# Optimization experiments

Measured on AMD Instinct MI355X. Metric: run time of the kernel, lower is better.

## Reference

```python
import jax, jax.numpy as jnp
import numpy as np

B, G, T, N = 2, 4, 64, 300
D = 256          # detr_dim == feature_dim
R = 4            # ffn_dim_ratio
MD = 32          # motion_dim


def _xavier(key, shape):
    lim = (6.0 / (shape[0] + shape[1])) ** 0.5
    return jax.random.uniform(key, shape, jnp.float32, -lim, lim)


def setup_inputs() -> dict:
    key = jax.random.key(0)
    ks = jax.random.split(key, 16)
    feats = jax.random.normal(ks[0], (B, G, T, N, D), jnp.float32)
    boxes = jax.random.uniform(ks[1], (B, G, T, N, 4), jnp.float32)
    masks = jax.random.bernoulli(ks[2], 0.3, (B, G, T, N))
    # per-trajectory permutation of frame ids 0..T-1 (unique -> unambiguous scatter)
    u = jax.random.uniform(ks[3], (B, G, N, T))
    times = jnp.swapaxes(jnp.argsort(u, axis=-1).astype(jnp.int32), 2, 3)  # [B,G,T,N]
    return {
        'trajectory_features': feats,
        'trajectory_boxes': boxes,
        'trajectory_masks': masks,
        'trajectory_times': times,
        'adp_w1': _xavier(ks[4], (D, D * R)), 'adp_b1': jnp.zeros((D * R,), jnp.float32),
        'adp_w2': _xavier(ks[5], (D * R, D)), 'adp_b2': jnp.zeros((D,), jnp.float32),
        'norm_g': jnp.ones((D,), jnp.float32), 'norm_b': jnp.zeros((D,), jnp.float32),
        'mot_w1': _xavier(ks[6], (12, MD // 2)), 'mot_b1': jnp.zeros((MD // 2,), jnp.float32),
        'mot_w2': _xavier(ks[7], (MD // 2, MD)), 'mot_b2': jnp.zeros((MD,), jnp.float32),
        'fus_w1': _xavier(ks[8], (D + MD, D)), 'fus_b1': jnp.zeros((D,), jnp.float32),
        'fus_w2': _xavier(ks[9], (D, D)), 'fus_b2': jnp.zeros((D,), jnp.float32),
        'ffn_w1': _xavier(ks[10], (D, D * R)), 'ffn_b1': jnp.zeros((D * R,), jnp.float32),
        'ffn_w2': _xavier(ks[11], (D * R, D)), 'ffn_b2': jnp.zeros((D,), jnp.float32),
        'fnorm_g': jnp.ones((D,), jnp.float32), 'fnorm_b': jnp.zeros((D,), jnp.float32),
    }


def _ffn(x, w1, b1, w2, b2):
    return jax.nn.gelu(x @ w1 + b1, approximate=False) @ w2 + b2


def _ln(x, g, b):
    m = x.mean(-1, keepdims=True)
    v = ((x - m) ** 2).mean(-1, keepdims=True)
    return (x - m) / jnp.sqrt(v + 1e-5) * g + b


def _motion_features(boxes, masks, times, mot_w1, mot_b1, mot_w2, mot_b2):
    # boxes [B,G,T,N,4] -> trajectory-major [B,G,N,T,*]
    b_, g_, t_, n_ = masks.shape
    md = mot_b2.shape[0]
    bx = jnp.swapaxes(boxes, 2, 3)              # [B,G,N,T,4]
    valid = ~jnp.swapaxes(masks, 2, 3)          # [B,G,N,T]
    tm = jnp.swapaxes(times, 2, 3)              # [B,G,N,T]
    # sort valid entries first, by time (stable)
    order = jnp.argsort(jnp.where(valid, tm, t_ + 1), axis=-1)
    sb = jnp.take_along_axis(bx, order[..., None], axis=3)   # sorted boxes
    st = jnp.take_along_axis(tm, order, axis=-1)             # sorted times
    cnt = valid.sum(-1)                                      # [B,G,N]
    pos = jnp.arange(t_)
    in_count = pos[None, None, None, :] < cnt[..., None]
    dt = jnp.maximum(st - jnp.roll(st, 1, axis=-1), 1).astype(sb.dtype)[..., None]
    mask_v = ((pos >= 1)[None, None, None, :] & in_count)[..., None]
    vel = jnp.where(mask_v, (sb - jnp.roll(sb, 1, axis=3)) / dt, 0.0)
    mask_a = ((pos >= 2)[None, None, None, :] & in_count)[..., None]
    acc = jnp.where(mask_a, (vel - jnp.roll(vel, 1, axis=3)) / dt, 0.0)
    mv = jnp.concatenate([sb, vel, acc], axis=-1)            # [B,G,N,T,12]
    enc = jax.nn.gelu(mv @ mot_w1 + mot_b1, approximate=False) @ mot_w2 + mot_b2
    write = in_count & (cnt >= 2)[..., None] & (st < t_)
    frame = jnp.where(write, st, t_)                         # t_ -> dropped
    bi, gi, ni, ti = jnp.meshgrid(jnp.arange(b_), jnp.arange(g_), jnp.arange(n_),
                                  jnp.arange(t_), indexing='ij')
    out = jnp.zeros((b_, g_, t_, n_, md), sb.dtype)
    return out.at[bi, gi, frame, ni].set(enc, mode='drop')


def reference(trajectory_features, trajectory_boxes, trajectory_masks, trajectory_times,
              adp_w1, adp_b1, adp_w2, adp_b2, norm_g, norm_b,
              mot_w1, mot_b1, mot_w2, mot_b2,
              fus_w1, fus_b1, fus_w2, fus_b2,
              ffn_w1, ffn_b1, ffn_w2, ffn_b2, fnorm_g, fnorm_b):
    x = trajectory_features + _ffn(trajectory_features, adp_w1, adp_b1, adp_w2, adp_b2)
    x = _ln(x, norm_g, norm_b)
    motion = _motion_features(trajectory_boxes, trajectory_masks, trajectory_times,
                              mot_w1, mot_b1, mot_w2, mot_b2)
    cat = jnp.concatenate([x, motion], axis=-1)
    fused = jax.nn.gelu(cat @ fus_w1 + fus_b1, approximate=False) @ fus_w2 + fus_b2
    fused = fused + _ffn(fused, ffn_w1, ffn_b1, ffn_w2, ffn_b2)
    fused = _ln(fused, fnorm_g, fnorm_b)
    return fused, motion
```

## Files before the change

### kernel.cpp

```cpp
#include <hip/hip_runtime.h>

typedef __bf16 bf16x8 __attribute__((ext_vector_type(8)));
typedef __bf16 bf16x4 __attribute__((ext_vector_type(4)));
typedef float f32x4 __attribute__((ext_vector_type(4)));

namespace {

constexpr int T_ = 64;
constexpr int N_ = 300;
constexpr int MD_ = 32;
constexpr int BG_ = 8;
constexpr long MROWS_ = (long)BG_ * T_ * N_;
constexpr long FUSED_N = MROWS_ * 256;
constexpr int MB = 32;

constexpr long PA1 = 0;
constexpr long PA2 = 262144;
constexpr long PF1 = 524288;
constexpr long PF2 = 598016;
constexpr long PN1 = 663552;
constexpr long PN2 = 925696;

__device__ __forceinline__ float gelu_f(float x) {
  const float x2 = x * x;
  const float z2 = x * fmaf(x2, 0.07135481627f, 1.5957691216f);
  const float t = __builtin_amdgcn_rcpf(1.0f + __expf(z2));
  return x * (1.0f - t);
}

__device__ __forceinline__ float gelu_exact(float x) {
  return 0.5f * x * (1.0f + erff(x * 0.7071067811865476f));
}

__global__ void k_zero_flag(int* f) { *f = 0; }

__global__ void k_detect_mask(const unsigned char* __restrict__ m, int nbytes,
                              int* __restrict__ f) {
  int i = blockIdx.x * 256 + threadIdx.x;
  if (i < nbytes && (i & 3) != 0 && m[i] != 0) atomicOr(f, 1);
}

__global__ __launch_bounds__(256)
void k_motion(const float* __restrict__ boxes, const void* __restrict__ masks,
              const int* __restrict__ times,
              const float* __restrict__ mw1, const float* __restrict__ mb1,
              const float* __restrict__ mw2, const float* __restrict__ mb2,
              float* __restrict__ motion, const int* __restrict__ flagp) {
  __shared__ int slot[4][T_];
  __shared__ int sts[4][T_];
  __shared__ float sbx[4][T_][4];
  __shared__ float otile[4][T_][MD_];
  const int tid = threadIdx.x;
  const int w = tid >> 6, l = tid & 63;
  const int traj = blockIdx.x * 4 + w;
  const int bg = traj / N_, n = traj - bg * N_;
  const int isbool = *flagp;
  const long idx = ((long)bg * T_ + l) * N_ + n;
  const bool msk = isbool ? (((const unsigned char*)masks)[idx] != 0)
                          : (((const int*)masks)[idx] != 0);
  const bool valid = !msk;
  const int tm = times[idx];

  slot[w][l] = -1;
  sts[w][l] = 0;
  *(float4*)&sbx[w][l][0] = make_float4(0.f, 0.f, 0.f, 0.f);
  __syncthreads();
  if (valid) slot[w][tm] = l;
  __syncthreads();

  const int ot = slot[w][l];
  const bool vp = ot >= 0;
  const unsigned long long bal = __ballot(vp);
  const int cnt = __builtin_popcountll(bal);
  const int pos = __builtin_popcountll(bal & ((1ull << l) - 1ull));
  if (vp) {
    sts[w][pos] = l;
    const float4 bx = *(const float4*)(boxes + (((long)bg * T_ + ot) * N_ + n) * 4);
    *(float4*)&sbx[w][pos][0] = bx;
  }
  __syncthreads();

  const int stp = sts[w][l];
  const int stm1 = sts[w][(l + 63) & 63];
  const float4 sb = *(const float4*)&sbx[w][l][0];
  const float4 sbm = *(const float4*)&sbx[w][(l + 63) & 63][0];
  const float dt = (float)max(stp - stm1, 1);
  const float inv = 1.0f / dt;
  const bool okv = (l >= 1) && (l < cnt);
  float v0 = okv ? (sb.x - sbm.x) * inv : 0.f;
  float v1 = okv ? (sb.y - sbm.y) * inv : 0.f;
  float v2 = okv ? (sb.z - sbm.z) * inv : 0.f;
  float v3 = okv ? (sb.w - sbm.w) * inv : 0.f;
  const float p0 = __shfl_up(v0, 1, 64);
  const float p1 = __shfl_up(v1, 1, 64);
  const float p2 = __shfl_up(v2, 1, 64);
  const float p3 = __shfl_up(v3, 1, 64);
  const bool oka = (l >= 2) && (l < cnt);
  const float a0 = oka ? (v0 - p0) * inv : 0.f;
  const float a1 = oka ? (v1 - p1) * inv : 0.f;
  const float a2 = oka ? (v2 - p2) * inv : 0.f;
  const float a3 = oka ? (v3 - p3) * inv : 0.f;

  const float mv[12] = {sb.x, sb.y, sb.z, sb.w, v0, v1, v2, v3, a0, a1, a2, a3};
  float e1[16];
#pragma unroll
  for (int i = 0; i < 16; ++i) {
    float a = mb1[i];
#pragma unroll
    for (int c = 0; c < 12; ++c) a = fmaf(mv[c], mw1[c * 16 + i], a);
    e1[i] = gelu_exact(a);
  }
  float enc[32];
#pragma unroll
  for (int o = 0; o < 32; ++o) {
    float a = mb2[o];
#pragma unroll
    for (int i = 0; i < 16; ++i) a = fmaf(e1[i], mw2[i * 32 + o], a);
    enc[o] = a;
  }

#pragma unroll
  for (int c = 0; c < 32; c += 4)
    *(float4*)&otile[w][l][c] = make_float4(0.f, 0.f, 0.f, 0.f);
  __syncthreads();
  if (l < cnt && cnt >= 2) {
#pragma unroll
    for (int c = 0; c < 32; ++c) otile[w][stp][c] = enc[c];
  }
  __syncthreads();

  float* mbase = motion + ((long)bg * T_ * N_ + n) * MD_;
  const float4* srcv = (const float4*)&otile[w][l][0];
  float4* dstv = (float4*)(mbase + (long)l * N_ * MD_);
#pragma unroll
  for (int q = 0; q < 8; ++q) dstv[q] = srcv[q];
}

__global__ void k_pack(const float* __restrict__ W, __bf16* __restrict__ P,
                       int K, int NN) {
  int gid = blockIdx.x * 256 + threadIdx.x;
  int total = (K >> 5) * (NN >> 4) * 64;
  if (gid >= total) return;
  int l = gid & 63, f = gid >> 6;
  int NT = NN >> 4;
  int kb = f / NT, nt = f - kb * NT;
  int krow = kb * 32 + (l >> 4) * 8;
  int col = nt * 16 + (l & 15);
  bf16x8 v;
#pragma unroll
  for (int e = 0; e < 8; ++e) v[e] = (__bf16)W[(long)(krow + e) * NN + col];
  *(bf16x8*)(P + (long)gid * 8) = v;
}

template <int NKB, bool MOT, int NT>
__device__ __forceinline__ void produce_chunk(
    const char* regA, const char* regM, char* hb, const __bf16* pb1,
    const float* b1, int r, int wid, int l, int lr, int lk) {
  const int nt = r * 4 + wid;
  f32x4 t[2];
  {
    const float4 bv = *(const float4*)(b1 + r * 64 + wid * 16 + lk * 4);
#pragma unroll
    for (int rt = 0; rt < 2; ++rt) t[rt] = f32x4{bv.x, bv.y, bv.z, bv.w};
  }
  const __bf16* wp = pb1 + ((long)nt << 9) + (l << 3);
  bf16x8 w0 = *(const bf16x8*)(wp);
  bf16x8 w1 = w0;
  if (NKB > 1) w1 = *(const bf16x8*)(wp + ((long)NT << 9));
#pragma unroll
  for (int kb = 0; kb < NKB; ++kb) {
    const bf16x8 wf = (kb & 1) ? w1 : w0;
    if (kb + 2 < NKB) {
      const bf16x8 v = *(const bf16x8*)(wp + ((long)(kb + 2) * NT << 9));
      if (kb & 1) w1 = v; else w0 = v;
    }
    __builtin_amdgcn_s_setprio(1);
#pragma unroll
    for (int rt = 0; rt < 2; ++rt) {
      const int row = rt * 16 + lr;
      bf16x8 xf;
      if (MOT && kb == NKB - 1)
        xf = *(const bf16x8*)(regM + row * 64 + ((lk ^ (row & 3)) << 4));
      else
        xf = *(const bf16x8*)(regA + row * 512 +
                              ((((kb << 2) + lk) ^ (row & 7)) << 4));
      t[rt] = __builtin_amdgcn_mfma_f32_16x16x32_bf16(wf, xf, t[rt], 0, 0, 0);
    }
    __builtin_amdgcn_s_setprio(0);
  }
#pragma unroll
  for (int rt = 0; rt < 2; ++rt) {
    const int row = rt * 16 + lr;
    bf16x4 hv;
#pragma unroll
    for (int e = 0; e < 4; ++e) hv[e] = (__bf16)gelu_f(t[rt][e]);
    *(bf16x4*)(hb + row * 128 + ((wid * 32 + lk * 8) ^ ((row & 7) << 4))) = hv;
  }
}

__device__ __forceinline__ void consume_chunk(const char* hb,
                                              const __bf16* pb2, int kbg0,
                                              int l, int lr, int lk, int wn,
                                              f32x4 (&acc)[2][4]) {
  const __bf16* wp = pb2 + ((long)(kbg0 * 16 + wn * 4) << 9) + (l << 3);
#pragma unroll
  for (int kbl = 0; kbl < 2; ++kbl) {
    bf16x8 bw[4];
#pragma unroll
    for (int j = 0; j < 4; ++j)
      bw[j] = *(const bf16x8*)(wp + ((long)(kbl * 16 + j) << 9));
    bf16x8 a[2];
#pragma unroll
    for (int m = 0; m < 2; ++m) {
      const int row = m * 16 + lr;
      a[m] = *(const bf16x8*)(hb + row * 128 +
                              ((kbl * 64 + lk * 16) ^ ((row & 7) << 4)));
    }
    __builtin_amdgcn_s_setprio(1);
#pragma unroll
    for (int j = 0; j < 4; ++j)
#pragma unroll
      for (int m = 0; m < 2; ++m)
        acc[m][j] = __builtin_amdgcn_mfma_f32_16x16x32_bf16(a[m], bw[j],
                                                            acc[m][j], 0, 0, 0);
    __builtin_amdgcn_s_setprio(0);
  }
}

__global__ __launch_bounds__(256, 4)
void k_mfma(const float* __restrict__ feats, const float* __restrict__ motion,
            const __bf16* __restrict__ pw,
            const float* __restrict__ ba1, const float* __restrict__ ba2,
            const float* __restrict__ ng, const float* __restrict__ nb,
            const float* __restrict__ bf1, const float* __restrict__ bf2,
            const float* __restrict__ bn1, const float* __restrict__ bn2,
            const float* __restrict__ fg, const float* __restrict__ fb,
            float* __restrict__ out) {
  __shared__ __align__(16) char smem[27648];
  char* regA = smem;
  char* hb0 = smem + 16384;
  char* hb1 = smem + 20480;
  char* regM = smem + 24576;
  float* redp = (float*)(smem + 26624);

  const int tid = threadIdx.x;
  const int l = tid & 63, wid = tid >> 6;
  const int lr = l & 15, lk = l >> 4;
  const int wn = wid;
  const int colb = wn * 64;
  const long rowbase = (long)blockIdx.x * MB;

  const __bf16* pa1 = pw + PA1;
  const __bf16* pa2 = pw + PA2;
  const __bf16* pf1 = pw + PF1;
  const __bf16* pf2 = pw + PF2;
  const __bf16* pn1 = pw + PN1;
  const __bf16* pn2 = pw + PN2;

  auto ln_stats = [&](const f32x4 (&acc)[2][4], float (&mean)[2][4],
                      float (&rstd)[2][4]) {
    float s1[2][4], s2[2][4];
#pragma unroll
    for (int m = 0; m < 2; ++m)
#pragma unroll
      for (int e = 0; e < 4; ++e) { s1[m][e] = 0.f; s2[m][e] = 0.f; }
#pragma unroll
    for (int m = 0; m < 2; ++m)
#pragma unroll
      for (int j = 0; j < 4; ++j)
#pragma unroll
        for (int e = 0; e < 4; ++e) {
          s1[m][e] += acc[m][j][e];
          s2[m][e] += acc[m][j][e] * acc[m][j][e];
        }
#pragma unroll
    for (int o = 1; o < 16; o <<= 1)
#pragma unroll
      for (int m = 0; m < 2; ++m)
#pragma unroll
        for (int e = 0; e < 4; ++e) {
          s1[m][e] += __shfl_xor(s1[m][e], o);
          s2[m][e] += __shfl_xor(s2[m][e], o);
        }
    if (lr == 0) {
#pragma unroll
      for (int m = 0; m < 2; ++m)
#pragma unroll
        for (int e = 0; e < 4; ++e) {
          const int row = m * 16 + lk * 4 + e;
          redp[(row * 4 + wn) * 2 + 0] = s1[m][e];
          redp[(row * 4 + wn) * 2 + 1] = s2[m][e];
        }
    }
    __syncthreads();
#pragma unroll
    for (int m = 0; m < 2; ++m)
#pragma unroll
      for (int e = 0; e < 4; ++e) {
        const int row = m * 16 + lk * 4 + e;
        const float S1 = redp[(row * 4 + 0) * 2] + redp[(row * 4 + 1) * 2] +
                         redp[(row * 4 + 2) * 2] + redp[(row * 4 + 3) * 2];
        const float S2 = redp[(row * 4 + 0) * 2 + 1] + redp[(row * 4 + 1) * 2 + 1] +
                         redp[(row * 4 + 2) * 2 + 1] + redp[(row * 4 + 3) * 2 + 1];
        const float mu = S1 * (1.0f / 256.0f);
        const float var = S2 * (1.0f / 256.0f) - mu * mu;
        mean[m][e] = mu;
        rstd[m][e] = rsqrtf(var + 1e-5f);
      }
  };

  f32x4 acc2[2][4];
#pragma unroll
  for (int j = 0; j < 4; ++j) {
    const int col = colb + j * 16 + lr;
    const float bv = ba2[col];
#pragma unroll
    for (int m = 0; m < 2; ++m)
#pragma unroll
      for (int e = 0; e < 4; ++e) {
        const int row = m * 16 + lk * 4 + e;
        acc2[m][j][e] = bv + feats[(rowbase + row) * 256 + col];
      }
  }
#pragma unroll
  for (int it = 0; it < 4; ++it) {
    const int c = tid + it * 256;
    const int row = c >> 5, cc = c & 31;
    const float* src = feats + (rowbase + row) * 256 + cc * 8;
    bf16x8 v;
#pragma unroll
    for (int e = 0; e < 8; ++e) v[e] = (__bf16)src[e];
    *(bf16x8*)(regA + row * 512 + ((cc ^ (row & 7)) << 4)) = v;
  }
  __syncthreads();

  produce_chunk<8, false, 64>(regA, regM, hb0, pa1, ba1, 0, wid, l, lr, lk);
  __syncthreads();
#pragma unroll 1
  for (int r = 0; r < 16; ++r) {
    if (r < 15)
      produce_chunk<8, false, 64>(regA, regM, ((r + 1) & 1) ? hb1 : hb0, pa1,
                                  ba1, r + 1, wid, l, lr, lk);
    consume_chunk((r & 1) ? hb1 : hb0, pa2, r * 2, l, lr, lk, wn, acc2);
    __syncthreads();
  }

  {
    float mean[2][4], rstd[2][4];
    ln_stats(acc2, mean, rstd);
#pragma unroll
    for (int j = 0; j < 4; ++j) {
      const int col = colb + j * 16 + lr;
      const float gv = ng[col], bv = nb[col];
#pragma unroll
      for (int m = 0; m < 2; ++m)
#pragma unroll
        for (int e = 0; e < 4; ++e) {
          const int row = m * 16 + lk * 4 + e;
          const float v = (acc2[m][j][e] - mean[m][e]) * rstd[m][e] * gv + bv;
          *(__bf16*)(regA + row * 512 + (((col >> 3) ^ (row & 7)) << 4) +
                     ((col & 7) << 1)) = (__bf16)v;
        }
    }
    if (tid < 128) {
      const int row = tid >> 2, cc = tid & 3;
      const float* src = motion + (rowbase + row) * 32 + cc * 8;
      bf16x8 v;
#pragma unroll
      for (int e = 0; e < 8; ++e) v[e] = (__bf16)src[e];
      *(bf16x8*)(regM + row * 64 + ((cc ^ (row & 3)) << 4)) = v;
    }
  }
  __syncthreads();

  {
#pragma unroll
    for (int j = 0; j < 4; ++j) {
      const float bv = bf2[colb + j * 16 + lr];
#pragma unroll
      for (int m = 0; m < 2; ++m) acc2[m][j] = {bv, bv, bv, bv};
    }
    produce_chunk<9, true, 16>(regA, regM, hb0, pf1, bf1, 0, wid, l, lr, lk);
    __syncthreads();
#pragma unroll 1
    for (int r = 0; r < 4; ++r) {
      if (r < 3)
        produce_chunk<9, true, 16>(regA, regM, ((r + 1) & 1) ? hb1 : hb0, pf1,
                                   bf1, r + 1, wid, l, lr, lk);
      consume_chunk((r & 1) ? hb1 : hb0, pf2, r * 2, l, lr, lk, wn, acc2);
      __syncthreads();
    }
#pragma unroll
    for (int j = 0; j < 4; ++j) {
      const int col = colb + j * 16 + lr;
      const float bv = bn2[col];
#pragma unroll
      for (int m = 0; m < 2; ++m)
#pragma unroll
        for (int e = 0; e < 4; ++e) {
          const int row = m * 16 + lk * 4 + e;
          const float fv = acc2[m][j][e];
          *(__bf16*)(regA + row * 512 + (((col >> 3) ^ (row & 7)) << 4) +
                     ((col & 7) << 1)) = (__bf16)fv;
          acc2[m][j][e] = fv + bv;
        }
    }
  }
  __syncthreads();

  produce_chunk<8, false, 64>(regA, regM, hb0, pn1, bn1, 0, wid, l, lr, lk);
  __syncthreads();
#pragma unroll 1
  for (int r = 0; r < 16; ++r) {
    if (r < 15)
      produce_chunk<8, false, 64>(regA, regM, ((r + 1) & 1) ? hb1 : hb0, pn1,
                                  bn1, r + 1, wid, l, lr, lk);
    consume_chunk((r & 1) ? hb1 : hb0, pn2, r * 2, l, lr, lk, wn, acc2);
    __syncthreads();
  }

  {
    float mean[2][4], rstd[2][4];
    ln_stats(acc2, mean, rstd);
#pragma unroll
    for (int j = 0; j < 4; ++j) {
      const int col = colb + j * 16 + lr;
      const float gv = fg[col], bv = fb[col];
#pragma unroll
      for (int m = 0; m < 2; ++m)
#pragma unroll
        for (int e = 0; e < 4; ++e) {
          const int row = m * 16 + lk * 4 + e;
          out[(rowbase + row) * 256 + col] =
              (acc2[m][j][e] - mean[m][e]) * rstd[m][e] * gv + bv;
        }
    }
  }
}

}

extern "C" void kernel_launch(void* const* d_in, const int* in_sizes, int n_in,
                              void* d_out, int out_size, void* d_ws, size_t ws_size,
                              hipStream_t stream) {
  const float* feats = (const float*)d_in[0];
  const float* boxes = (const float*)d_in[1];
  const void*  masks = d_in[2];
  const int*   times = (const int*)d_in[3];
  const float* wa1 = (const float*)d_in[4];
  const float* ba1 = (const float*)d_in[5];
  const float* wa2 = (const float*)d_in[6];
  const float* ba2 = (const float*)d_in[7];
  const float* ng  = (const float*)d_in[8];
  const float* nb  = (const float*)d_in[9];
  const float* mw1 = (const float*)d_in[10];
  const float* mb1 = (const float*)d_in[11];
  const float* mw2 = (const float*)d_in[12];
  const float* mb2 = (const float*)d_in[13];
  const float* wf1 = (const float*)d_in[14];
  const float* bf1 = (const float*)d_in[15];
  const float* wf2 = (const float*)d_in[16];
  const float* bf2 = (const float*)d_in[17];
  const float* wn1 = (const float*)d_in[18];
  const float* bn1 = (const float*)d_in[19];
  const float* wn2 = (const float*)d_in[20];
  const float* bn2 = (const float*)d_in[21];
  const float* fg  = (const float*)d_in[22];
  const float* fb  = (const float*)d_in[23];

  float* out_fused = (float*)d_out;
  float* out_motion = out_fused + FUSED_N;
  int* flag = (int*)d_ws;
  __bf16* pw = (__bf16*)((char*)d_ws + 256);

  const int mask_elems = in_sizes[2];

  k_zero_flag<<<1, 1, 0, stream>>>(flag);
  k_detect_mask<<<(mask_elems + 255) / 256, 256, 0, stream>>>(
      (const unsigned char*)masks, mask_elems, flag);
  k_motion<<<(BG_ * N_) / 4, 256, 0, stream>>>(boxes, masks, times, mw1, mb1, mw2,
                                               mb2, out_motion, flag);

  auto packn = [&](const float* W, long off, int K, int NN) {
    const int total = (K / 32) * (NN / 16) * 64;
    k_pack<<<(total + 255) / 256, 256, 0, stream>>>(W, pw + off, K, NN);
  };
  packn(wa1, PA1, 256, 1024);
  packn(wa2, PA2, 1024, 256);
  packn(wf1, PF1, 288, 256);
  packn(wf2, PF2, 256, 256);
  packn(wn1, PN1, 256, 1024);
  packn(wn2, PN2, 1024, 256);

  k_mfma<<<(int)(MROWS_ / MB), 256, 0, stream>>>(
      feats, out_motion, pw, ba1, ba2, ng, nb, bf1, bf2, bn1, bn2, fg, fb,
      out_fused);
}
```

Measured before the change: 604.5 us.

## Warp-specialize fused MLP kernel into producer and consumer wavefronts

Doubles the block to 512 threads and splits the wavefronts by role. Four waves compute the first GEMM plus GELU into the double-buffered LDS chunk, and four waves hold the accumulators and run the second GEMM, the residual and the LayerNorm. Producer and consumer work now run concurrently on separate waves instead of being interleaved within each wave. In exchange, each block uses more threads and half the waves sit idle during the non-GEMM phases. The launch bound of 512 threads with 4 blocks may also squeeze registers.

```diff
diff --git a/kernel.cpp b/kernel.cpp
--- a/kernel.cpp
+++ b/kernel.cpp
@@ -155,11 +155,11 @@
 template <int NKB, bool MOT, int NT>
 __device__ __forceinline__ void produce_chunk(
     const char* regA, const char* regM, char* hb, const __bf16* pb1,
-    const float* b1, int r, int wid, int l, int lr, int lk) {
-  const int nt = r * 4 + wid;
+    const float* b1, int r, int pw, int l, int lr, int lk) {
+  const int nt = r * 4 + pw;
   f32x4 t[2];
   {
-    const float4 bv = *(const float4*)(b1 + r * 64 + wid * 16 + lk * 4);
+    const float4 bv = *(const float4*)(b1 + r * 64 + pw * 16 + lk * 4);
 #pragma unroll
     for (int rt = 0; rt < 2; ++rt) t[rt] = f32x4{bv.x, bv.y, bv.z, bv.w};
   }
@@ -194,7 +194,7 @@
     bf16x4 hv;
 #pragma unroll
     for (int e = 0; e < 4; ++e) hv[e] = (__bf16)gelu_f(t[rt][e]);
-    *(bf16x4*)(hb + row * 128 + ((wid * 32 + lk * 8) ^ ((row & 7) << 4))) = hv;
+    *(bf16x4*)(hb + row * 128 + ((pw * 32 + lk * 8) ^ ((row & 7) << 4))) = hv;
   }
 }
 
@@ -227,7 +227,7 @@
   }
 }
 
-__global__ __launch_bounds__(256, 4)
+__global__ __launch_bounds__(512, 4)
 void k_mfma(const float* __restrict__ feats, const float* __restrict__ motion,
             const __bf16* __restrict__ pw,
             const float* __restrict__ ba1, const float* __restrict__ ba2,
@@ -246,8 +246,9 @@
   const int tid = threadIdx.x;
   const int l = tid & 63, wid = tid >> 6;
   const int lr = l & 15, lk = l >> 4;
-  const int wn = wid;
-  const int colb = wn * 64;
+  const bool prod = wid >= 4;
+  const int pw4 = wid & 3;
+  const int colb = pw4 * 64;
   const long rowbase = (long)blockIdx.x * MB;
 
   const __bf16* pa1 = pw + PA1;
@@ -257,74 +258,24 @@
   const __bf16* pn1 = pw + PN1;
   const __bf16* pn2 = pw + PN2;
 
-  auto ln_stats = [&](const f32x4 (&acc)[2][4], float (&mean)[2][4],
-                      float (&rstd)[2][4]) {
-    float s1[2][4], s2[2][4];
-#pragma unroll
-    for (int m = 0; m < 2; ++m)
-#pragma unroll
-      for (int e = 0; e < 4; ++e) { s1[m][e] = 0.f; s2[m][e] = 0.f; }
-#pragma unroll
-    for (int m = 0; m < 2; ++m)
-#pragma unroll
-      for (int j = 0; j < 4; ++j)
-#pragma unroll
-        for (int e = 0; e < 4; ++e) {
-          s1[m][e] += acc[m][j][e];
-          s2[m][e] += acc[m][j][e] * acc[m][j][e];
-        }
-#pragma unroll
-    for (int o = 1; o < 16; o <<= 1)
-#pragma unroll
-      for (int m = 0; m < 2; ++m)
-#pragma unroll
-        for (int e = 0; e < 4; ++e) {
-          s1[m][e] += __shfl_xor(s1[m][e], o);
-          s2[m][e] += __shfl_xor(s2[m][e], o);
-        }
-    if (lr == 0) {
+  f32x4 acc2[2][4];
+  if (!prod) {
+#pragma unroll
+    for (int j = 0; j < 4; ++j) {
+      const int col = colb + j * 16 + lr;
+      const float bv = ba2[col];
 #pragma unroll
       for (int m = 0; m < 2; ++m)
 #pragma unroll
         for (int e = 0; e < 4; ++e) {
           const int row = m * 16 + lk * 4 + e;
-          redp[(row * 4 + wn) * 2 + 0] = s1[m][e];
-          redp[(row * 4 + wn) * 2 + 1] = s2[m][e];
+          acc2[m][j][e] = bv + feats[(rowbase + row) * 256 + col];
         }
     }
-    __syncthreads();
-#pragma unroll
-    for (int m = 0; m < 2; ++m)
-#pragma unroll
-      for (int e = 0; e < 4; ++e) {
-        const int row = m * 16 + lk * 4 + e;
-        const float S1 = redp[(row * 4 + 0) * 2] + redp[(row * 4 + 1) * 2] +
-                         redp[(row * 4 + 2) * 2] + redp[(row * 4 + 3) * 2];
-        const float S2 = redp[(row * 4 + 0) * 2 + 1] + redp[(row * 4 + 1) * 2 + 1] +
-                         redp[(row * 4 + 2) * 2 + 1] + redp[(row * 4 + 3) * 2 + 1];
-        const float mu = S1 * (1.0f / 256.0f);
-        const float var = S2 * (1.0f / 256.0f) - mu * mu;
-        mean[m][e] = mu;
-        rstd[m][e] = rsqrtf(var + 1e-5f);
-      }
-  };
-
-  f32x4 acc2[2][4];
-#pragma unroll
-  for (int j = 0; j < 4; ++j) {
-    const int col = colb + j * 16 + lr;
-    const float bv = ba2[col];
-#pragma unroll
-    for (int m = 0; m < 2; ++m)
-#pragma unroll
-      for (int e = 0; e < 4; ++e) {
-        const int row = m * 16 + lk * 4 + e;
-        acc2[m][j][e] = bv + feats[(rowbase + row) * 256 + col];
-      }
-  }
-#pragma unroll
-  for (int it = 0; it < 4; ++it) {
-    const int c = tid + it * 256;
+  }
+#pragma unroll
+  for (int it = 0; it < 2; ++it) {
+    const int c = tid + it * 512;
     const int row = c >> 5, cc = c & 31;
     const float* src = feats + (rowbase + row) * 256 + cc * 8;
     bf16x8 v;
@@ -334,36 +285,93 @@
   }
   __syncthreads();
 
-  produce_chunk<8, false, 64>(regA, regM, hb0, pa1, ba1, 0, wid, l, lr, lk);
+  if (prod)
+    produce_chunk<8, false, 64>(regA, regM, hb0, pa1, ba1, 0, pw4, l, lr, lk);
   __syncthreads();
 #pragma unroll 1
   for (int r = 0; r < 16; ++r) {
-    if (r < 15)
-      produce_chunk<8, false, 64>(regA, regM, ((r + 1) & 1) ? hb1 : hb0, pa1,
-                                  ba1, r + 1, wid, l, lr, lk);
-    consume_chunk((r & 1) ? hb1 : hb0, pa2, r * 2, l, lr, lk, wn, acc2);
+    if (prod) {
+      if (r < 15)
+        produce_chunk<8, false, 64>(regA, regM, ((r + 1) & 1) ? hb1 : hb0, pa1,
+                                    ba1, r + 1, pw4, l, lr, lk);
+    } else {
+      consume_chunk((r & 1) ? hb1 : hb0, pa2, r * 2, l, lr, lk, pw4, acc2);
+    }
     __syncthreads();
   }
 
   {
     float mean[2][4], rstd[2][4];
-    ln_stats(acc2, mean, rstd);
-#pragma unroll
-    for (int j = 0; j < 4; ++j) {
-      const int col = colb + j * 16 + lr;
-      const float gv = ng[col], bv = nb[col];
+    if (!prod) {
+      float s1[2][4], s2[2][4];
+#pragma unroll
+      for (int m = 0; m < 2; ++m)
+#pragma unroll
+        for (int e = 0; e < 4; ++e) { s1[m][e] = 0.f; s2[m][e] = 0.f; }
+#pragma unroll
+      for (int m = 0; m < 2; ++m)
+#pragma unroll
+        for (int j = 0; j < 4; ++j)
+#pragma unroll
+          for (int e = 0; e < 4; ++e) {
+            s1[m][e] += acc2[m][j][e];
+            s2[m][e] += acc2[m][j][e] * acc2[m][j][e];
+          }
+#pragma unroll
+      for (int o = 1; o < 16; o <<= 1)
+#pragma unroll
+        for (int m = 0; m < 2; ++m)
+#pragma unroll
+          for (int e = 0; e < 4; ++e) {
+            s1[m][e] += __shfl_xor(s1[m][e], o);
+            s2[m][e] += __shfl_xor(s2[m][e], o);
+          }
+      if (lr == 0) {
+#pragma unroll
+        for (int m = 0; m < 2; ++m)
+#pragma unroll
+          for (int e = 0; e < 4; ++e) {
+            const int row = m * 16 + lk * 4 + e;
+            redp[(row * 4 + pw4) * 2 + 0] = s1[m][e];
+            redp[(row * 4 + pw4) * 2 + 1] = s2[m][e];
+          }
+      }
+    }
+    __syncthreads();
+    if (!prod) {
 #pragma unroll
       for (int m = 0; m < 2; ++m)
 #pragma unroll
         for (int e = 0; e < 4; ++e) {
           const int row = m * 16 + lk * 4 + e;
-          const float v = (acc2[m][j][e] - mean[m][e]) * rstd[m][e] * gv + bv;
-          *(__bf16*)(regA + row * 512 + (((col >> 3) ^ (row & 7)) << 4) +
-                     ((col & 7) << 1)) = (__bf16)v;
+          const float S1 = redp[(row * 4 + 0) * 2] + redp[(row * 4 + 1) * 2] +
+                           redp[(row * 4 + 2) * 2] + redp[(row * 4 + 3) * 2];
+          const float S2 = redp[(row * 4 + 0) * 2 + 1] +
+                           redp[(row * 4 + 1) * 2 + 1] +
+                           redp[(row * 4 + 2) * 2 + 1] +
+                           redp[(row * 4 + 3) * 2 + 1];
+          const float mu = S1 * (1.0f / 256.0f);
+          const float var = S2 * (1.0f / 256.0f) - mu * mu;
+          mean[m][e] = mu;
+          rstd[m][e] = rsqrtf(var + 1e-5f);
         }
-    }
-    if (tid < 128) {
-      const int row = tid >> 2, cc = tid & 3;
+#pragma unroll
+      for (int j = 0; j < 4; ++j) {
+        const int col = colb + j * 16 + lr;
+        const float gv = ng[col], bv = nb[col];
+#pragma unroll
+        for (int m = 0; m < 2; ++m)
+#pragma unroll
+          for (int e = 0; e < 4; ++e) {
+            const int row = m * 16 + lk * 4 + e;
+            const float v = (acc2[m][j][e] - mean[m][e]) * rstd[m][e] * gv + bv;
+            *(__bf16*)(regA + row * 512 + (((col >> 3) ^ (row & 7)) << 4) +
+                       ((col & 7) << 1)) = (__bf16)v;
+          }
+      }
+    } else if (tid < 384) {
+      const int c = tid - 256;
+      const int row = c >> 2, cc = c & 3;
       const float* src = motion + (rowbase + row) * 32 + cc * 8;
       bf16x8 v;
 #pragma unroll
@@ -374,65 +382,121 @@
   __syncthreads();
 
   {
-#pragma unroll
-    for (int j = 0; j < 4; ++j) {
-      const float bv = bf2[colb + j * 16 + lr];
-#pragma unroll
-      for (int m = 0; m < 2; ++m) acc2[m][j] = {bv, bv, bv, bv};
-    }
-    produce_chunk<9, true, 16>(regA, regM, hb0, pf1, bf1, 0, wid, l, lr, lk);
+    if (!prod) {
+#pragma unroll
+      for (int j = 0; j < 4; ++j) {
+        const float bv = bf2[colb + j * 16 + lr];
+#pragma unroll
+        for (int m = 0; m < 2; ++m) acc2[m][j] = {bv, bv, bv, bv};
+      }
+    }
+    if (prod)
+      produce_chunk<9, true, 16>(regA, regM, hb0, pf1, bf1, 0, pw4, l, lr, lk);
     __syncthreads();
 #pragma unroll 1
     for (int r = 0; r < 4; ++r) {
-      if (r < 3)
-        produce_chunk<9, true, 16>(regA, regM, ((r + 1) & 1) ? hb1 : hb0, pf1,
-                                   bf1, r + 1, wid, l, lr, lk);
-      consume_chunk((r & 1) ? hb1 : hb0, pf2, r * 2, l, lr, lk, wn, acc2);
+      if (prod) {
+        if (r < 3)
+          produce_chunk<9, true, 16>(regA, regM, ((r + 1) & 1) ? hb1 : hb0, pf1,
+                                     bf1, r + 1, pw4, l, lr, lk);
+      } else {
+        consume_chunk((r & 1) ? hb1 : hb0, pf2, r * 2, l, lr, lk, pw4, acc2);
+      }
       __syncthreads();
     }
-#pragma unroll
-    for (int j = 0; j < 4; ++j) {
-      const int col = colb + j * 16 + lr;
-      const float bv = bn2[col];
+    if (!prod) {
+#pragma unroll
+      for (int j = 0; j < 4; ++j) {
+        const int col = colb + j * 16 + lr;
+        const float bv = bn2[col];
+#pragma unroll
+        for (int m = 0; m < 2; ++m)
+#pragma unroll
+          for (int e = 0; e < 4; ++e) {
+            const int row = m * 16 + lk * 4 + e;
+            const float fv = acc2[m][j][e];
+            *(__bf16*)(regA + row * 512 + (((col >> 3) ^ (row & 7)) << 4) +
+                       ((col & 7) << 1)) = (__bf16)fv;
+            acc2[m][j][e] = fv + bv;
+          }
+      }
+    }
+  }
+  __syncthreads();
+
+  if (prod)
+    produce_chunk<8, false, 64>(regA, regM, hb0, pn1, bn1, 0, pw4, l, lr, lk);
+  __syncthreads();
+#pragma unroll 1
+  for (int r = 0; r < 16; ++r) {
+    if (prod) {
+      if (r < 15)
+        produce_chunk<8, false, 64>(regA, regM, ((r + 1) & 1) ? hb1 : hb0, pn1,
+                                    bn1, r + 1, pw4, l, lr, lk);
+    } else {
+      consume_chunk((r & 1) ? hb1 : hb0, pn2, r * 2, l, lr, lk, pw4, acc2);
+    }
+    __syncthreads();
+  }
+
+  {
+    if (!prod) {
+      float s1[2][4], s2[2][4];
+#pragma unroll
+      for (int m = 0; m < 2; ++m)
+#pragma unroll
+        for (int e = 0; e < 4; ++e) { s1[m][e] = 0.f; s2[m][e] = 0.f; }
+#pragma unroll
+      for (int m = 0; m < 2; ++m)
+#pragma unroll
+        for (int j = 0; j < 4; ++j)
+#pragma unroll
+          for (int e = 0; e < 4; ++e) {
+            s1[m][e] += acc2[m][j][e];
+            s2[m][e] += acc2[m][j][e] * acc2[m][j][e];
+          }
+#pragma unroll
+      for (int o = 1; o < 16; o <<= 1)
+#pragma unroll
+        for (int m = 0; m < 2; ++m)
+#pragma unroll
+          for (int e = 0; e < 4; ++e) {
+            s1[m][e] += __shfl_xor(s1[m][e], o);
+            s2[m][e] += __shfl_xor(s2[m][e], o);
+          }
+      if (lr == 0) {
+#pragma unroll
+        for (int m = 0; m < 2; ++m)
+#pragma unroll
+          for (int e = 0; e < 4; ++e) {
+            const int row = m * 16 + lk * 4 + e;
+            redp[(row * 4 + pw4) * 2 + 0] = s1[m][e];
+            redp[(row * 4 + pw4) * 2 + 1] = s2[m][e];
+          }
+      }
+    }
+    __syncthreads();
+    if (!prod) {
 #pragma unroll
       for (int m = 0; m < 2; ++m)
 #pragma unroll
         for (int e = 0; e < 4; ++e) {
           const int row = m * 16 + lk * 4 + e;
-          const float fv = acc2[m][j][e];
-          *(__bf16*)(regA + row * 512 + (((col >> 3) ^ (row & 7)) << 4) +
-                     ((col & 7) << 1)) = (__bf16)fv;
-          acc2[m][j][e] = fv + bv;
-        }
-    }
-  }
-  __syncthreads();
-
-  produce_chunk<8, false, 64>(regA, regM, hb0, pn1, bn1, 0, wid, l, lr, lk);
-  __syncthreads();
-#pragma unroll 1
-  for (int r = 0; r < 16; ++r) {
-    if (r < 15)
-      produce_chunk<8, false, 64>(regA, regM, ((r + 1) & 1) ? hb1 : hb0, pn1,
-                                  bn1, r + 1, wid, l, lr, lk);
-    consume_chunk((r & 1) ? hb1 : hb0, pn2, r * 2, l, lr, lk, wn, acc2);
-    __syncthreads();
-  }
-
-  {
-    float mean[2][4], rstd[2][4];
-    ln_stats(acc2, mean, rstd);
-#pragma unroll
-    for (int j = 0; j < 4; ++j) {
-      const int col = colb + j * 16 + lr;
-      const float gv = fg[col], bv = fb[col];
-#pragma unroll
-      for (int m = 0; m < 2; ++m)
-#pragma unroll
-        for (int e = 0; e < 4; ++e) {
-          const int row = m * 16 + lk * 4 + e;
-          out[(rowbase + row) * 256 + col] =
-              (acc2[m][j][e] - mean[m][e]) * rstd[m][e] * gv + bv;
+          const float S1 = redp[(row * 4 + 0) * 2] + redp[(row * 4 + 1) * 2] +
+                           redp[(row * 4 + 2) * 2] + redp[(row * 4 + 3) * 2];
+          const float S2 = redp[(row * 4 + 0) * 2 + 1] +
+                           redp[(row * 4 + 1) * 2 + 1] +
+                           redp[(row * 4 + 2) * 2 + 1] +
+                           redp[(row * 4 + 3) * 2 + 1];
+          const float mu = S1 * (1.0f / 256.0f);
+          const float var = S2 * (1.0f / 256.0f) - mu * mu;
+          const float rs = rsqrtf(var + 1e-5f);
+#pragma unroll
+          for (int j = 0; j < 4; ++j) {
+            const int col = colb + j * 16 + lr;
+            out[(rowbase + row) * 256 + col] =
+                (acc2[m][j][e] - mu) * rs * fg[col] + fb[col];
+          }
         }
     }
   }
@@ -471,7 +535,7 @@
   float* out_fused = (float*)d_out;
   float* out_motion = out_fused + FUSED_N;
   int* flag = (int*)d_ws;
-  __bf16* pw = (__bf16*)((char*)d_ws + 256);
+  __bf16* pwp = (__bf16*)((char*)d_ws + 256);
 
   const int mask_elems = in_sizes[2];
 
@@ -483,7 +547,7 @@
 
   auto packn = [&](const float* W, long off, int K, int NN) {
     const int total = (K / 32) * (NN / 16) * 64;
-    k_pack<<<(total + 255) / 256, 256, 0, stream>>>(W, pw + off, K, NN);
+    k_pack<<<(total + 255) / 256, 256, 0, stream>>>(W, pwp + off, K, NN);
   };
   packn(wa1, PA1, 256, 1024);
   packn(wa2, PA2, 1024, 256);
@@ -492,7 +556,7 @@
   packn(wn1, PN1, 256, 1024);
   packn(wn2, PN2, 1024, 256);
 
-  k_mfma<<<(int)(MROWS_ / MB), 256, 0, stream>>>(
-      feats, out_motion, pw, ba1, ba2, ng, nb, bf1, bf2, bn1, bn2, fg, fb,
+  k_mfma<<<(int)(MROWS_ / MB), 512, 0, stream>>>(
+      feats, out_motion, pwp, ba1, ba2, ng, nb, bf1, bf2, bn1, bn2, fg, fb,
       out_fused);
 }
```

Result: slower. 714.5 us (+18.2%).

## Double hidden chunk width to 128 columns per produce/consume step

Applied to the files above, without the earlier changes.

Each produce step now has every wave compute two 16-column hidden tiles instead of one, so a chunk is 128 hidden columns. Each consume step covers four k-blocks instead of two, which halves the number of pipeline iterations and __syncthreads barriers in all three FFN stages, and each A fragment from LDS now feeds two MFMAs. The cost is larger LDS hidden buffers (shared memory grows to about 35 KB) and more registers. The launch bound drops from 4 to 3 blocks per CU, so occupancy may fall.

```diff
diff --git a/kernel.cpp b/kernel.cpp
--- a/kernel.cpp
+++ b/kernel.cpp
@@ -156,23 +156,31 @@
 __device__ __forceinline__ void produce_chunk(
     const char* regA, const char* regM, char* hb, const __bf16* pb1,
     const float* b1, int r, int wid, int l, int lr, int lk) {
-  const int nt = r * 4 + wid;
-  f32x4 t[2];
-  {
-    const float4 bv = *(const float4*)(b1 + r * 64 + wid * 16 + lk * 4);
-#pragma unroll
-    for (int rt = 0; rt < 2; ++rt) t[rt] = f32x4{bv.x, bv.y, bv.z, bv.w};
-  }
-  const __bf16* wp = pb1 + ((long)nt << 9) + (l << 3);
-  bf16x8 w0 = *(const bf16x8*)(wp);
-  bf16x8 w1 = w0;
-  if (NKB > 1) w1 = *(const bf16x8*)(wp + ((long)NT << 9));
+  const int nt0 = r * 8 + wid * 2;
+  f32x4 t[2][2];
+#pragma unroll
+  for (int n = 0; n < 2; ++n) {
+    const float4 bv = *(const float4*)(b1 + (nt0 + n) * 16 + lk * 4);
+    t[n][0] = f32x4{bv.x, bv.y, bv.z, bv.w};
+    t[n][1] = t[n][0];
+  }
+  const __bf16* wp0 = pb1 + ((long)nt0 << 9) + (l << 3);
+  const __bf16* wp1 = wp0 + (1 << 9);
+  bf16x8 wa0 = *(const bf16x8*)(wp0);
+  bf16x8 wa1 = *(const bf16x8*)(wp1);
+  bf16x8 wb0 = wa0, wb1 = wa1;
+  if (NKB > 1) {
+    wb0 = *(const bf16x8*)(wp0 + ((long)NT << 9));
+    wb1 = *(const bf16x8*)(wp1 + ((long)NT << 9));
+  }
 #pragma unroll
   for (int kb = 0; kb < NKB; ++kb) {
-    const bf16x8 wf = (kb & 1) ? w1 : w0;
+    const bf16x8 wf0 = (kb & 1) ? wb0 : wa0;
+    const bf16x8 wf1 = (kb & 1) ? wb1 : wa1;
     if (kb + 2 < NKB) {
-      const bf16x8 v = *(const bf16x8*)(wp + ((long)(kb + 2) * NT << 9));
-      if (kb & 1) w1 = v; else w0 = v;
+      const bf16x8 v0 = *(const bf16x8*)(wp0 + ((long)((kb + 2) * NT) << 9));
+      const bf16x8 v1 = *(const bf16x8*)(wp1 + ((long)((kb + 2) * NT) << 9));
+      if (kb & 1) { wb0 = v0; wb1 = v1; } else { wa0 = v0; wa1 = v1; }
     }
     __builtin_amdgcn_s_setprio(1);
 #pragma unroll
@@ -184,18 +192,22 @@
       else
         xf = *(const bf16x8*)(regA + row * 512 +
                               ((((kb << 2) + lk) ^ (row & 7)) << 4));
-      t[rt] = __builtin_amdgcn_mfma_f32_16x16x32_bf16(wf, xf, t[rt], 0, 0, 0);
+      t[0][rt] = __builtin_amdgcn_mfma_f32_16x16x32_bf16(wf0, xf, t[0][rt], 0, 0, 0);
+      t[1][rt] = __builtin_amdgcn_mfma_f32_16x16x32_bf16(wf1, xf, t[1][rt], 0, 0, 0);
     }
     __builtin_amdgcn_s_setprio(0);
   }
 #pragma unroll
-  for (int rt = 0; rt < 2; ++rt) {
-    const int row = rt * 16 + lr;
-    bf16x4 hv;
-#pragma unroll
-    for (int e = 0; e < 4; ++e) hv[e] = (__bf16)gelu_f(t[rt][e]);
-    *(bf16x4*)(hb + row * 128 + ((wid * 32 + lk * 8) ^ ((row & 7) << 4))) = hv;
-  }
+  for (int n = 0; n < 2; ++n)
+#pragma unroll
+    for (int rt = 0; rt < 2; ++rt) {
+      const int row = rt * 16 + lr;
+      bf16x4 hv;
+#pragma unroll
+      for (int e = 0; e < 4; ++e) hv[e] = (__bf16)gelu_f(t[n][rt][e]);
+      *(bf16x4*)(hb + row * 256 +
+                 ((wid * 64 + n * 32 + lk * 8) ^ ((row & 7) << 4))) = hv;
+    }
 }
 
 __device__ __forceinline__ void consume_chunk(const char* hb,
@@ -204,7 +216,7 @@
                                               f32x4 (&acc)[2][4]) {
   const __bf16* wp = pb2 + ((long)(kbg0 * 16 + wn * 4) << 9) + (l << 3);
 #pragma unroll
-  for (int kbl = 0; kbl < 2; ++kbl) {
+  for (int kbl = 0; kbl < 4; ++kbl) {
     bf16x8 bw[4];
 #pragma unroll
     for (int j = 0; j < 4; ++j)
@@ -213,7 +225,7 @@
 #pragma unroll
     for (int m = 0; m < 2; ++m) {
       const int row = m * 16 + lr;
-      a[m] = *(const bf16x8*)(hb + row * 128 +
+      a[m] = *(const bf16x8*)(hb + row * 256 +
                               ((kbl * 64 + lk * 16) ^ ((row & 7) << 4)));
     }
     __builtin_amdgcn_s_setprio(1);
@@ -227,7 +239,7 @@
   }
 }
 
-__global__ __launch_bounds__(256, 4)
+__global__ __launch_bounds__(256, 3)
 void k_mfma(const float* __restrict__ feats, const float* __restrict__ motion,
             const __bf16* __restrict__ pw,
             const float* __restrict__ ba1, const float* __restrict__ ba2,
@@ -236,12 +248,12 @@
             const float* __restrict__ bn1, const float* __restrict__ bn2,
             const float* __restrict__ fg, const float* __restrict__ fb,
             float* __restrict__ out) {
-  __shared__ __align__(16) char smem[27648];
+  __shared__ __align__(16) char smem[35840];
   char* regA = smem;
   char* hb0 = smem + 16384;
-  char* hb1 = smem + 20480;
-  char* regM = smem + 24576;
-  float* redp = (float*)(smem + 26624);
+  char* hb1 = smem + 24576;
+  char* regM = smem + 32768;
+  float* redp = (float*)(smem + 34816);
 
   const int tid = threadIdx.x;
   const int l = tid & 63, wid = tid >> 6;
@@ -337,11 +349,11 @@
   produce_chunk<8, false, 64>(regA, regM, hb0, pa1, ba1, 0, wid, l, lr, lk);
   __syncthreads();
 #pragma unroll 1
-  for (int r = 0; r < 16; ++r) {
-    if (r < 15)
+  for (int r = 0; r < 8; ++r) {
+    if (r < 7)
       produce_chunk<8, false, 64>(regA, regM, ((r + 1) & 1) ? hb1 : hb0, pa1,
                                   ba1, r + 1, wid, l, lr, lk);
-    consume_chunk((r & 1) ? hb1 : hb0, pa2, r * 2, l, lr, lk, wn, acc2);
+    consume_chunk((r & 1) ? hb1 : hb0, pa2, r * 4, l, lr, lk, wn, acc2);
     __syncthreads();
   }
 
@@ -382,14 +394,11 @@
     }
     produce_chunk<9, true, 16>(regA, regM, hb0, pf1, bf1, 0, wid, l, lr, lk);
     __syncthreads();
-#pragma unroll 1
-    for (int r = 0; r < 4; ++r) {
-      if (r < 3)
-        produce_chunk<9, true, 16>(regA, regM, ((r + 1) & 1) ? hb1 : hb0, pf1,
-                                   bf1, r + 1, wid, l, lr, lk);
-      consume_chunk((r & 1) ? hb1 : hb0, pf2, r * 2, l, lr, lk, wn, acc2);
-      __syncthreads();
-    }
+    produce_chunk<9, true, 16>(regA, regM, hb1, pf1, bf1, 1, wid, l, lr, lk);
+    consume_chunk(hb0, pf2, 0, l, lr, lk, wn, acc2);
+    __syncthreads();
+    consume_chunk(hb1, pf2, 4, l, lr, lk, wn, acc2);
+    __syncthreads();
 #pragma unroll
     for (int j = 0; j < 4; ++j) {
       const int col = colb + j * 16 + lr;
@@ -411,11 +420,11 @@
   produce_chunk<8, false, 64>(regA, regM, hb0, pn1, bn1, 0, wid, l, lr, lk);
   __syncthreads();
 #pragma unroll 1
-  for (int r = 0; r < 16; ++r) {
-    if (r < 15)
+  for (int r = 0; r < 8; ++r) {
+    if (r < 7)
       produce_chunk<8, false, 64>(regA, regM, ((r + 1) & 1) ? hb1 : hb0, pn1,
                                   bn1, r + 1, wid, l, lr, lk);
-    consume_chunk((r & 1) ? hb1 : hb0, pn2, r * 2, l, lr, lk, wn, acc2);
+    consume_chunk((r & 1) ? hb1 : hb0, pn2, r * 4, l, lr, lk, wn, acc2);
     __syncthreads();
   }
 
@@ -471,7 +480,7 @@
   float* out_fused = (float*)d_out;
   float* out_motion = out_fused + FUSED_N;
   int* flag = (int*)d_ws;
-  __bf16* pw = (__bf16*)((char*)d_ws + 256);
+  __bf16* pwp = (__bf16*)((char*)d_ws + 256);
 
   const int mask_elems = in_sizes[2];
 
@@ -483,7 +492,7 @@
 
   auto packn = [&](const float* W, long off, int K, int NN) {
     const int total = (K / 32) * (NN / 16) * 64;
-    k_pack<<<(total + 255) / 256, 256, 0, stream>>>(W, pw + off, K, NN);
+    k_pack<<<(total + 255) / 256, 256, 0, stream>>>(W, pwp + off, K, NN);
   };
   packn(wa1, PA1, 256, 1024);
   packn(wa2, PA2, 1024, 256);
@@ -493,6 +502,6 @@
   packn(wn2, PN2, 1024, 256);
 
   k_mfma<<<(int)(MROWS_ / MB), 256, 0, stream>>>(
-      feats, out_motion, pw, ba1, ba2, ng, nb, bf1, bf2, bn1, bn2, fg, fb,
+      feats, out_motion, pwp, ba1, ba2, ng, nb, bf1, bf2, bn1, bn2, fg, fb,
       out_fused);
 }
```

Result: faster. 568.3 us (-6.0%).
